# Performance work log

Measured on AMD Instinct MI355X. Metric: run time of the kernel, lower is better.

Reference implementation:

```python
import jax, jax.numpy as jnp
import numpy as np

EPS = 1e-05
H, N, F = 1024, 16, 4096  # hidden_dim, state_dim, ffn_dim


def layernorm(x, g, b):
    mu = jnp.mean(x, axis=-1, keepdims=True)
    var = jnp.mean(jnp.square(x - mu), axis=-1, keepdims=True)
    return (x - mu) * jax.lax.rsqrt(var + EPS) * g + b


def setup_inputs() -> dict:
    key = jax.random.key(0)
    ks = jax.random.split(key, 12)
    B, L = 2, 2048
    s = lambda fan_in: 1.0 / np.sqrt(fan_in)
    inp = {
        "x": jax.random.normal(ks[0], (B, L, H), jnp.float32),
        "ln1_g": jnp.ones((H,), jnp.float32),
        "ln1_b": jnp.zeros((H,), jnp.float32),
        "Wd": jax.random.uniform(ks[1], (H, H), jnp.float32, -s(H), s(H)),
        "bd": jnp.zeros((H,), jnp.float32),
        "Wbc": jax.random.uniform(ks[2], (2 * N, H), jnp.float32, -s(H), s(H)),
        "bbc": jnp.zeros((2 * N,), jnp.float32),
        "A_log": jnp.log(jnp.tile(jnp.arange(1, N + 1, dtype=jnp.float32), (H, 1))),
        "D": jnp.ones((H,), jnp.float32),
        "ln2_g": jnp.ones((H,), jnp.float32),
        "ln2_b": jnp.zeros((H,), jnp.float32),
        "W1": jax.random.uniform(ks[3], (F, H), jnp.float32, -s(H), s(H)),
        "b1": jnp.zeros((F,), jnp.float32),
        "W2": jax.random.uniform(ks[4], (H, F), jnp.float32, -s(F), s(F)),
        "b2": jnp.zeros((H,), jnp.float32),
    }
    return inp


def _selective_ssm(xn, delta, Bm, Cm, A, D):
    # xn: (B,L,H)  delta: (B,L,H)  Bm,Cm: (B,L,N)  A: (H,N)  D: (H,)
    Bsz = xn.shape[0]
    # time-major for scan
    xs = (jnp.moveaxis(delta, 1, 0), jnp.moveaxis(Bm, 1, 0),
          jnp.moveaxis(Cm, 1, 0), jnp.moveaxis(xn, 1, 0))

    def step(h, t):
        d_t, b_t, c_t, x_t = t  # (B,H), (B,N), (B,N), (B,H)
        dA = jnp.exp(d_t[:, :, None] * A)                      # (B,H,N)
        dBx = d_t[:, :, None] * b_t[:, None, :] * x_t[:, :, None]
        h = dA * h + dBx                                       # (B,H,N)
        y = jnp.einsum('bhn,bn->bh', h, c_t)                   # (B,H)
        return h, y

    h0 = jnp.zeros((Bsz, H, N), xn.dtype)
    _, ys = jax.lax.scan(step, h0, xs)
    y = jnp.moveaxis(ys, 0, 1)  # (B,L,H)
    return y + D * xn


def reference(x, ln1_g, ln1_b, Wd, bd, Wbc, bbc, A_log, D,
              ln2_g, ln2_b, W1, b1, W2, b2):
    # --- SSMLayer: pre-norm selective SSM + residual ---
    xn = layernorm(x, ln1_g, ln1_b)
    delta = jax.nn.softplus(xn @ Wd.T + bd)      # (B,L,H)
    bc = xn @ Wbc.T + bbc                        # (B,L,2N)
    Bm, Cm = bc[..., :N], bc[..., N:]
    A = -jnp.exp(A_log)                          # (H,N), negative real
    ssm_out = x + _selective_ssm(xn, delta, Bm, Cm, A, D)
    # --- MambaBlock: norm -> FFN -> residual with ssm_out ---
    normed = layernorm(ssm_out, ln2_g, ln2_b)
    hff = jax.nn.gelu(normed @ W1.T + b1, approximate=False)
    ffn_out = hff @ W2.T + b2
    return ffn_out + ssm_out
```

## Files before the change

### kernel.cpp

```cpp
#include <hip/hip_runtime.h>
#include <cstdint>
#include <cstddef>

typedef unsigned short USHORT;
typedef __bf16 bf16x8 __attribute__((ext_vector_type(8)));
typedef float f32x4 __attribute__((ext_vector_type(4)));

__device__ __forceinline__ float b2f(USHORT u) {
    union { unsigned int i; float f; } v; v.i = ((unsigned int)u) << 16; return v.f;
}
__device__ __forceinline__ USHORT f2bf(float f) {
    union { float f; unsigned int i; } v; v.f = f;
    unsigned int u = v.i;
    unsigned int r = (u + 0x7FFFu + ((u >> 16) & 1u)) >> 16;
    return (USHORT)r;
}
__device__ __forceinline__ float fexp2(float x) { return __builtin_amdgcn_exp2f(x); }

__device__ __forceinline__ void gload_lds16(const void* g, void* l) {
    __builtin_amdgcn_global_load_lds(
        (const __attribute__((address_space(1))) void*)(uintptr_t)g,
        (__attribute__((address_space(3))) void*)(uint32_t)(uintptr_t)l,
        16, 0, 0);
}

__global__ __launch_bounds__(256)
void f2b_kernel(const float* __restrict__ src, USHORT* __restrict__ dst, int n)
{
    int i = (blockIdx.x * 256 + threadIdx.x) * 4;
    if (i < n) {
        float4 v = *(const float4*)(src + i);
        ushort4 o;
        o.x = f2bf(v.x); o.y = f2bf(v.y); o.z = f2bf(v.z); o.w = f2bf(v.w);
        *(ushort4*)(dst + i) = o;
    }
}

__global__ __launch_bounds__(256)
void ln_kernel(const float* __restrict__ inp, const float* __restrict__ g,
               const float* __restrict__ bsh, USHORT* __restrict__ out)
{
    const int tid = threadIdx.x;
    const size_t row = blockIdx.x;
    float4 t = ((const float4*)inp)[row * 256 + tid];
    float v[4] = { t.x, t.y, t.z, t.w };
    float s = v[0] + v[1] + v[2] + v[3];
    float sq = v[0]*v[0] + v[1]*v[1] + v[2]*v[2] + v[3]*v[3];
    #pragma unroll
    for (int off = 32; off; off >>= 1) { s += __shfl_down(s, off); sq += __shfl_down(sq, off); }
    __shared__ float red[8];
    const int wv = tid >> 6;
    if ((tid & 63) == 0) { red[wv] = s; red[wv + 4] = sq; }
    __syncthreads();
    const float S  = red[0] + red[1] + red[2] + red[3];
    const float SQ = red[4] + red[5] + red[6] + red[7];
    const float mu = S * (1.0f / 1024.0f);
    const float var = SQ * (1.0f / 1024.0f) - mu * mu;
    const float rs = rsqrtf(var + 1e-5f);
    float4 gv = ((const float4*)g)[tid];
    float4 bv = ((const float4*)bsh)[tid];
    ushort4 o;
    o.x = f2bf((v[0] - mu) * rs * gv.x + bv.x);
    o.y = f2bf((v[1] - mu) * rs * gv.y + bv.y);
    o.z = f2bf((v[2] - mu) * rs * gv.z + bv.z);
    o.w = f2bf((v[3] - mu) * rs * gv.w + bv.w);
    ((ushort4*)out)[row * 256 + tid] = o;
}

template<int EPI>
__global__ __launch_bounds__(256)
void gemm_bt(const USHORT* __restrict__ A, const USHORT* __restrict__ B,
             const float* __restrict__ bias, void* __restrict__ outp,
             void* __restrict__ outp2, int M, int N, int K, int lda, int ldb)
{
    __shared__ __align__(16) unsigned char smem[32768];
    USHORT* As = (USHORT*)smem;
    USHORT* Bs = (USHORT*)(smem + 8192);
    const int tid = threadIdx.x;
    const int lane = tid & 63;
    const int w = tid >> 6;
    const int wr = w >> 1, wc = w & 1;

    const int nx = gridDim.x, ny = gridDim.y;
    const int pid = blockIdx.y * nx + blockIdx.x;
    const int npg = 8 * nx;
    const int gid = pid / npg;
    const int first = gid * 8;
    const int rem = ny - first;
    const int gsz = (rem < 8) ? rem : 8;
    const int py = first + (pid % npg) % gsz;
    const int px = (pid % npg) / gsz;
    const int tm = py * 128;
    const int tn = px * 128;

    USHORT* po = nullptr;
    if constexpr (EPI == 3) {
        const int z = blockIdx.z;
        A += (size_t)z * K;
        B += (size_t)z * K;
        po = ((z < 2) ? (USHORT*)outp : (USHORT*)outp2) + (size_t)(z & 1) * M * N;
    }

    f32x4 acc[4][4];
    #pragma unroll
    for (int i = 0; i < 4; i++)
        #pragma unroll
        for (int j = 0; j < 4; j++) acc[i][j] = (f32x4){0.f, 0.f, 0.f, 0.f};

    const int srow = tid >> 2;
    const int scol = (tid & 3) * 8;
    const USHORT* gA0 = A + (size_t)(tm + srow) * lda + scol;
    const USHORT* gA1 = A + (size_t)(tm + 64 + srow) * lda + scol;
    const USHORT* gB0 = B + (size_t)(tn + srow) * ldb + scol;
    const USHORT* gB1 = B + (size_t)(tn + 64 + srow) * ldb + scol;
    USHORT* lA0 = As + w * 512;
    USHORT* lA1 = As + 2048 + w * 512;
    USHORT* lB0 = Bs + w * 512;
    USHORT* lB1 = Bs + 2048 + w * 512;

    const int fr = lane & 15;
    const int fko = (lane >> 4) * 8;
    const int quad = lane >> 4;

    for (int k0 = 0; k0 < K; k0 += 64) {
        gload_lds16(gA0 + k0, lA0);
        gload_lds16(gA1 + k0, lA1);
        gload_lds16(gB0 + k0, lB0);
        gload_lds16(gB1 + k0, lB1);
        gload_lds16(gA0 + k0 + 32, lA0 + 8192);
        gload_lds16(gA1 + k0 + 32, lA1 + 8192);
        gload_lds16(gB0 + k0 + 32, lB0 + 8192);
        gload_lds16(gB1 + k0 + 32, lB1 + 8192);
        __syncthreads();
        #pragma unroll
        for (int h = 0; h < 2; h++) {
            const USHORT* Ah = As + h * 8192;
            const USHORT* Bh = Bs + h * 8192;
            bf16x8 af[4], bfr[4];
            #pragma unroll
            for (int i = 0; i < 4; i++) {
                af[i]  = *(const bf16x8*)(Ah + (wr * 64 + i * 16 + fr) * 32 + fko);
                bfr[i] = *(const bf16x8*)(Bh + (wc * 64 + i * 16 + fr) * 32 + fko);
            }
            #pragma unroll
            for (int i = 0; i < 4; i++)
                #pragma unroll
                for (int j = 0; j < 4; j++)
                    acc[i][j] = __builtin_amdgcn_mfma_f32_16x16x32_bf16(af[i], bfr[j], acc[i][j], 0, 0, 0);
        }
        __syncthreads();
    }

    float* eW = (float*)(smem + (size_t)w * 4352);
    const int rr = lane >> 5;
    const int cc = lane & 31;
    const int gcolb = tn + wc * 64;
    float2 bvv;
    if constexpr (EPI == 3) { bvv.x = 0.f; bvv.y = 0.f; }
    else bvv = *(const float2*)&bias[gcolb + cc * 2];

    #pragma unroll
    for (int i = 0; i < 4; i++) {
        #pragma unroll
        for (int j = 0; j < 4; j++)
            #pragma unroll
            for (int r = 0; r < 4; r++)
                eW[(quad * 4 + r) * 68 + j * 16 + fr] = acc[i][j][r];
        __syncthreads();
        const int grow0 = tm + wr * 64 + i * 16;
        #pragma unroll
        for (int rp = 0; rp < 8; rp++) {
            const int row = rp * 2 + rr;
            const float2 v = *(const float2*)&eW[row * 68 + cc * 2];
            const size_t gidx = (size_t)(grow0 + row) * N + gcolb + cc * 2;
            if constexpr (EPI == 1) {
                const float z0 = v.x + bvv.x, z1 = v.y + bvv.y;
                const float u0 = z0 * (0.7978845608f + 0.035677408f * z0 * z0);
                const float u1 = z1 * (0.7978845608f + 0.035677408f * z1 * z1);
                const float s0 = __builtin_amdgcn_rcpf(1.f + fexp2(2.885390082f * u0));
                const float s1 = __builtin_amdgcn_rcpf(1.f + fexp2(2.885390082f * u1));
                const float g0 = z0 * (1.f - s0), g1 = z1 * (1.f - s1);
                const uint32_t pk = (uint32_t)f2bf(g0) | ((uint32_t)f2bf(g1) << 16);
                *(uint32_t*)((USHORT*)outp + gidx) = pk;
            } else {
                const uint32_t pk = (uint32_t)f2bf(v.x) | ((uint32_t)f2bf(v.y) << 16);
                *(uint32_t*)(po + gidx) = pk;
            }
        }
        __syncthreads();
    }
}

__global__ __launch_bounds__(256)
void delta_reduce(const USHORT* __restrict__ p, const float* __restrict__ bias,
                  float* __restrict__ out)
{
    const size_t PS = (size_t)4096 * 1024;
    const size_t i = ((size_t)blockIdx.x * 256 + threadIdx.x) * 4;
    ushort4 a = *(const ushort4*)(p + i);
    ushort4 b = *(const ushort4*)(p + PS + i);
    float4 bv = *(const float4*)(bias + (i & 1023));
    float z[4] = { b2f(a.x) + b2f(b.x) + bv.x, b2f(a.y) + b2f(b.y) + bv.y,
                   b2f(a.z) + b2f(b.z) + bv.z, b2f(a.w) + b2f(b.w) + bv.w };
    float4 o;
    o.x = (z[0] > 20.f) ? z[0] : 0.69314718f * __log2f(1.f + fexp2(z[0] * 1.44269504f));
    o.y = (z[1] > 20.f) ? z[1] : 0.69314718f * __log2f(1.f + fexp2(z[1] * 1.44269504f));
    o.z = (z[2] > 20.f) ? z[2] : 0.69314718f * __log2f(1.f + fexp2(z[2] * 1.44269504f));
    o.w = (z[3] > 20.f) ? z[3] : 0.69314718f * __log2f(1.f + fexp2(z[3] * 1.44269504f));
    *(float4*)(out + i) = o;
}

__global__ __launch_bounds__(256)
void ffn2_reduce(const USHORT* __restrict__ p01, const USHORT* __restrict__ p23,
                 const float* __restrict__ bias, const float* __restrict__ extra,
                 float* __restrict__ out)
{
    const size_t PS = (size_t)4096 * 1024;
    const size_t i = ((size_t)blockIdx.x * 256 + threadIdx.x) * 4;
    ushort4 a = *(const ushort4*)(p01 + i);
    ushort4 b = *(const ushort4*)(p01 + PS + i);
    ushort4 c = *(const ushort4*)(p23 + i);
    ushort4 d = *(const ushort4*)(p23 + PS + i);
    float4 bv = *(const float4*)(bias + (i & 1023));
    float4 ev = *(const float4*)(extra + i);
    float4 o;
    o.x = b2f(a.x) + b2f(b.x) + b2f(c.x) + b2f(d.x) + bv.x + ev.x;
    o.y = b2f(a.y) + b2f(b.y) + b2f(c.y) + b2f(d.y) + bv.y + ev.y;
    o.z = b2f(a.z) + b2f(b.z) + b2f(c.z) + b2f(d.z) + bv.z + ev.z;
    o.w = b2f(a.w) + b2f(b.w) + b2f(c.w) + b2f(d.w) + bv.w + ev.w;
    *(float4*)(out + i) = o;
}

__global__ __launch_bounds__(256)
void bc_mfma(const USHORT* __restrict__ xn, const USHORT* __restrict__ WbcB,
             const float* __restrict__ bbc, float* __restrict__ bc)
{
    __shared__ __align__(16) USHORT As[64 * 32];
    __shared__ __align__(16) USHORT Bs[32 * 32];
    const int tid = threadIdx.x;
    const int lane = tid & 63;
    const int w = tid >> 6;
    const int tok0 = blockIdx.x * 64;

    const int srow = tid >> 2;
    const int scol = (tid & 3) * 8;
    const USHORT* gA = xn + (size_t)(tok0 + srow) * 1024 + scol;
    const USHORT* gB = WbcB + (size_t)srow * 1024 + scol;
    USHORT* lA = As + w * 512;
    USHORT* lB = Bs + w * 512;

    const int fr = lane & 15;
    const int fko = (lane >> 4) * 8;
    const int quad = lane >> 4;

    f32x4 acc[2];
    acc[0] = (f32x4){0.f, 0.f, 0.f, 0.f};
    acc[1] = (f32x4){0.f, 0.f, 0.f, 0.f};

    for (int k0 = 0; k0 < 1024; k0 += 32) {
        gload_lds16(gA + k0, lA);
        if (w < 2) gload_lds16(gB + k0, lB);
        __syncthreads();
        bf16x8 af = *(const bf16x8*)(As + (w * 16 + fr) * 32 + fko);
        bf16x8 b0 = *(const bf16x8*)(Bs + (fr) * 32 + fko);
        bf16x8 b1 = *(const bf16x8*)(Bs + (16 + fr) * 32 + fko);
        acc[0] = __builtin_amdgcn_mfma_f32_16x16x32_bf16(af, b0, acc[0], 0, 0, 0);
        acc[1] = __builtin_amdgcn_mfma_f32_16x16x32_bf16(af, b1, acc[1], 0, 0, 0);
        __syncthreads();
    }

    #pragma unroll
    for (int j = 0; j < 2; j++) {
        const int col = j * 16 + fr;
        const float bv = bbc[col];
        #pragma unroll
        for (int r = 0; r < 4; r++) {
            const int row = tok0 + w * 16 + quad * 4 + r;
            bc[(size_t)row * 32 + col] = acc[j][r] + bv;
        }
    }
}

#define SCAN_P 64
#define SCAN_T 32

__global__ __launch_bounds__(256)
void scan_pass1(const USHORT* __restrict__ xn, const float* __restrict__ delta,
                const float* __restrict__ bc, const float* __restrict__ Alog,
                float* __restrict__ sEnd, float* __restrict__ Ptot)
{
    const int tid = threadIdx.x;
    const int h = blockIdx.x * 256 + tid;
    const int b = blockIdx.y;
    const int p = blockIdx.z;
    const size_t tok0 = (size_t)b * 2048 + p * SCAN_T;

    __shared__ __align__(16) float sBC[SCAN_T][32];
    {
        int t = tid >> 3, q = (tid & 7) * 4;
        *(float4*)&sBC[t][q] = *(const float4*)(bc + (tok0 + t) * 32 + q);
    }

    float en[16], s[16], P[16];
    #pragma unroll
    for (int k = 0; k < 4; k++) {
        float4 a = *(const float4*)(Alog + h * 16 + k * 4);
        en[k*4+0] = -__expf(a.x) * 1.44269504f;
        en[k*4+1] = -__expf(a.y) * 1.44269504f;
        en[k*4+2] = -__expf(a.z) * 1.44269504f;
        en[k*4+3] = -__expf(a.w) * 1.44269504f;
    }
    #pragma unroll
    for (int n = 0; n < 16; n++) { s[n] = 0.f; P[n] = 1.f; }
    __syncthreads();

    const float* dp = delta + tok0 * 1024 + h;
    const USHORT* xp = xn + tok0 * 1024 + h;
    float d_c = dp[0];
    USHORT x_c = xp[0];
    for (int t = 0; t < SCAN_T; ++t) {
        const int tn = (t < SCAN_T - 1) ? t + 1 : t;
        float d_n = dp[(size_t)tn * 1024];
        USHORT x_n = xp[(size_t)tn * 1024];
        const float dx = d_c * b2f(x_c);
        #pragma unroll
        for (int k = 0; k < 4; k++) {
            float4 Bv = *(const float4*)&sBC[t][k*4];
            float bb[4] = { Bv.x, Bv.y, Bv.z, Bv.w };
            #pragma unroll
            for (int j = 0; j < 4; j++) {
                const int n = k*4 + j;
                const float dA = fexp2(d_c * en[n]);
                s[n] = fmaf(dA, s[n], dx * bb[j]);
                P[n] *= dA;
            }
        }
        d_c = d_n; x_c = x_n;
    }

    const size_t off = (size_t)p * 32768 + ((size_t)b * 1024 + h) * 16;
    #pragma unroll
    for (int k = 0; k < 4; k++) {
        *(float4*)(sEnd + off + k*4) = (float4){ s[k*4], s[k*4+1], s[k*4+2], s[k*4+3] };
        *(float4*)(Ptot + off + k*4) = (float4){ P[k*4], P[k*4+1], P[k*4+2], P[k*4+3] };
    }
}

__global__ __launch_bounds__(256)
void scan_mid(const float* __restrict__ sEnd, const float* __restrict__ Ptot,
              float* __restrict__ sIn)
{
    const int L = blockIdx.x * 256 + threadIdx.x;
    float s = 0.f;
    #pragma unroll 8
    for (int p = 0; p < SCAN_P; ++p) {
        const size_t off = (size_t)p * 32768 + L;
        sIn[off] = s;
        s = fmaf(Ptot[off], s, sEnd[off]);
    }
}

__global__ __launch_bounds__(256)
void scan_pass2(const float* __restrict__ x, const USHORT* __restrict__ xn,
                const float* __restrict__ delta, const float* __restrict__ bc,
                const float* __restrict__ Alog, const float* __restrict__ Dp,
                const float* __restrict__ sIn, float* __restrict__ ssm)
{
    const int tid = threadIdx.x;
    const int h = blockIdx.x * 256 + tid;
    const int b = blockIdx.y;
    const int p = blockIdx.z;
    const size_t tok0 = (size_t)b * 2048 + p * SCAN_T;

    __shared__ __align__(16) float sBC[SCAN_T][32];
    {
        int t = tid >> 3, q = (tid & 7) * 4;
        *(float4*)&sBC[t][q] = *(const float4*)(bc + (tok0 + t) * 32 + q);
    }

    float en[16], s[16];
    #pragma unroll
    for (int k = 0; k < 4; k++) {
        float4 a = *(const float4*)(Alog + h * 16 + k * 4);
        en[k*4+0] = -__expf(a.x) * 1.44269504f;
        en[k*4+1] = -__expf(a.y) * 1.44269504f;
        en[k*4+2] = -__expf(a.z) * 1.44269504f;
        en[k*4+3] = -__expf(a.w) * 1.44269504f;
    }
    const size_t off = (size_t)p * 32768 + ((size_t)b * 1024 + h) * 16;
    #pragma unroll
    for (int k = 0; k < 4; k++) {
        float4 v = *(const float4*)(sIn + off + k*4);
        s[k*4] = v.x; s[k*4+1] = v.y; s[k*4+2] = v.z; s[k*4+3] = v.w;
    }
    const float Dv = Dp[h];
    __syncthreads();

    const float* dp = delta + tok0 * 1024 + h;
    const USHORT* xp = xn + tok0 * 1024 + h;
    const float* xrp = x + tok0 * 1024 + h;
    float* op = ssm + tok0 * 1024 + h;

    float d_c = dp[0];
    USHORT x_c = xp[0];
    float xr_c = xrp[0];
    for (int t = 0; t < SCAN_T; ++t) {
        const int tn = (t < SCAN_T - 1) ? t + 1 : t;
        float d_n = dp[(size_t)tn * 1024];
        USHORT x_n = xp[(size_t)tn * 1024];
        float xr_n = xrp[(size_t)tn * 1024];
        const float xv = b2f(x_c);
        const float dx = d_c * xv;
        float y = 0.f;
        #pragma unroll
        for (int k = 0; k < 4; k++) {
            float4 Bv = *(const float4*)&sBC[t][k*4];
            float4 Cv = *(const float4*)&sBC[t][16 + k*4];
            float bb[4] = { Bv.x, Bv.y, Bv.z, Bv.w };
            float cc[4] = { Cv.x, Cv.y, Cv.z, Cv.w };
            #pragma unroll
            for (int j = 0; j < 4; j++) {
                const int n = k*4 + j;
                const float dA = fexp2(d_c * en[n]);
                s[n] = fmaf(dA, s[n], dx * bb[j]);
                y = fmaf(cc[j], s[n], y);
            }
        }
        op[(size_t)t * 1024] = xr_c + y + Dv * xv;
        d_c = d_n; x_c = x_n; xr_c = xr_n;
    }
}

extern "C" void kernel_launch(void* const* d_in, const int* in_sizes, int n_in,
                              void* d_out, int out_size, void* d_ws, size_t ws_size,
                              hipStream_t stream)
{
    const float* x    = (const float*)d_in[0];
    const float* ln1g = (const float*)d_in[1];
    const float* ln1b = (const float*)d_in[2];
    const float* Wd   = (const float*)d_in[3];
    const float* bd   = (const float*)d_in[4];
    const float* Wbc  = (const float*)d_in[5];
    const float* bbc  = (const float*)d_in[6];
    const float* Alog = (const float*)d_in[7];
    const float* Dp   = (const float*)d_in[8];
    const float* ln2g = (const float*)d_in[9];
    const float* ln2b = (const float*)d_in[10];
    const float* W1   = (const float*)d_in[11];
    const float* b1   = (const float*)d_in[12];
    const float* W2   = (const float*)d_in[13];
    const float* b2   = (const float*)d_in[14];
    float* out = (float*)d_out;

    char* ws = (char*)d_ws;
    const size_t MB = 1024 * 1024;
    float*  deltaW = (float*)(ws + 0);
    float*  ssmW   = (float*)(ws + 16 * MB);
    USHORT* xnW    = (USHORT*)(ws + 32 * MB);
    USHORT* nrmW   = (USHORT*)(ws + 40 * MB);
    USHORT* hffW   = (USHORT*)(ws + 48 * MB);
    float*  bcW    = (float*)(ws + 80 * MB);
    USHORT* WdB    = (USHORT*)(ws + 81 * MB);
    USHORT* W1B    = (USHORT*)(ws + 83 * MB);
    USHORT* W2B    = (USHORT*)(ws + 91 * MB);
    USHORT* WbcB   = (USHORT*)(ws + 99 * MB);
    USHORT* dpart  = (USHORT*)(ws + 48 * MB);
    float*  sEndW  = (float*)(ws + 48 * MB);
    float*  PtotW  = (float*)(ws + 56 * MB);
    float*  sInW   = (float*)(ws + 64 * MB);
    USHORT* ffn2p01 = (USHORT*)(ws + 0);
    USHORT* ffn2p23 = (USHORT*)(ws + 32 * MB);

    f2b_kernel<<<1024, 256, 0, stream>>>(Wd, WdB, 1024 * 1024);
    f2b_kernel<<<4096, 256, 0, stream>>>(W1, W1B, 4096 * 1024);
    f2b_kernel<<<4096, 256, 0, stream>>>(W2, W2B, 1024 * 4096);
    f2b_kernel<<<32, 256, 0, stream>>>(Wbc, WbcB, 32 * 1024);
    ln_kernel<<<4096, 256, 0, stream>>>(x, ln1g, ln1b, xnW);
    gemm_bt<3><<<dim3(8, 32, 2), 256, 0, stream>>>(xnW, WdB, nullptr, dpart, nullptr, 4096, 1024, 512, 1024, 1024);
    delta_reduce<<<4096, 256, 0, stream>>>(dpart, bd, deltaW);
    bc_mfma<<<64, 256, 0, stream>>>(xnW, WbcB, bbc, bcW);
    scan_pass1<<<dim3(4, 2, SCAN_P), 256, 0, stream>>>(xnW, deltaW, bcW, Alog, sEndW, PtotW);
    scan_mid<<<128, 256, 0, stream>>>(sEndW, PtotW, sInW);
    scan_pass2<<<dim3(4, 2, SCAN_P), 256, 0, stream>>>(x, xnW, deltaW, bcW, Alog, Dp, sInW, ssmW);
    ln_kernel<<<4096, 256, 0, stream>>>(ssmW, ln2g, ln2b, nrmW);
    gemm_bt<1><<<dim3(32, 32), 256, 0, stream>>>(nrmW, W1B, b1, hffW, nullptr, 4096, 4096, 1024, 1024, 1024);
    gemm_bt<3><<<dim3(8, 32, 4), 256, 0, stream>>>(hffW, W2B, nullptr, ffn2p01, ffn2p23, 4096, 1024, 1024, 4096, 4096);
    ffn2_reduce<<<4096, 256, 0, stream>>>(ffn2p01, ffn2p23, b2, ssmW, out);

    (void)in_sizes; (void)n_in; (void)out_size; (void)ws_size;
}
```

Before: 333.3 us.

## Store split-K partials in MFMA fragment layout and merge weight conversion launches

The split-K GEMM epilogue no longer stages accumulators through LDS with block barriers. Each lane writes its accumulators as packed bf16 pairs straight into a tiled, fragment-ordered buffer. The delta and FFN2 reduce kernels are rewritten to decode that tiled layout, and the four weight-conversion launches become one kernel. The GELU epilogue also drops its per-block barriers, since each wave only touches its own LDS region. In return, the reduce kernels read 32-bit words of which they use only one 16-bit half, relying on cache reuse between neighbouring rows.

```diff
diff --git a/kernel.cpp b/kernel.cpp
--- a/kernel.cpp
+++ b/kernel.cpp
@@ -25,15 +25,22 @@
 }
 
 __global__ __launch_bounds__(256)
-void f2b_kernel(const float* __restrict__ src, USHORT* __restrict__ dst, int n)
-{
-    int i = (blockIdx.x * 256 + threadIdx.x) * 4;
-    if (i < n) {
-        float4 v = *(const float4*)(src + i);
-        ushort4 o;
-        o.x = f2bf(v.x); o.y = f2bf(v.y); o.z = f2bf(v.z); o.w = f2bf(v.w);
-        *(ushort4*)(dst + i) = o;
-    }
+void f2b_all(const float* __restrict__ Wd, const float* __restrict__ W1,
+             const float* __restrict__ W2, const float* __restrict__ Wbc,
+             USHORT* __restrict__ WdB, USHORT* __restrict__ W1B,
+             USHORT* __restrict__ W2B, USHORT* __restrict__ WbcB)
+{
+    const int bid = blockIdx.x;
+    const float* src; USHORT* dst; int off;
+    if (bid < 1024)      { src = Wd;  dst = WdB;  off = bid; }
+    else if (bid < 5120) { src = W1;  dst = W1B;  off = bid - 1024; }
+    else if (bid < 9216) { src = W2;  dst = W2B;  off = bid - 5120; }
+    else                 { src = Wbc; dst = WbcB; off = bid - 9216; }
+    const int i = (off * 256 + threadIdx.x) * 4;
+    float4 v = *(const float4*)(src + i);
+    ushort4 o;
+    o.x = f2bf(v.x); o.y = f2bf(v.y); o.z = f2bf(v.z); o.w = f2bf(v.w);
+    *(ushort4*)(dst + i) = o;
 }
 
 __global__ __launch_bounds__(256)
@@ -93,12 +100,13 @@
     const int tm = py * 128;
     const int tn = px * 128;
 
-    USHORT* po = nullptr;
+    uint32_t* po = nullptr;
     if constexpr (EPI == 3) {
         const int z = blockIdx.z;
         A += (size_t)z * K;
         B += (size_t)z * K;
-        po = ((z < 2) ? (USHORT*)outp : (USHORT*)outp2) + (size_t)(z & 1) * M * N;
+        USHORT* p16 = ((z < 2) ? (USHORT*)outp : (USHORT*)outp2) + (size_t)(z & 1) * M * N;
+        po = (uint32_t*)p16;
     }
 
     f32x4 acc[4][4];
@@ -151,29 +159,40 @@
         __syncthreads();
     }
 
-    float* eW = (float*)(smem + (size_t)w * 4352);
-    const int rr = lane >> 5;
-    const int cc = lane & 31;
-    const int gcolb = tn + wc * 64;
-    float2 bvv;
-    if constexpr (EPI == 3) { bvv.x = 0.f; bvv.y = 0.f; }
-    else bvv = *(const float2*)&bias[gcolb + cc * 2];
-
-    #pragma unroll
-    for (int i = 0; i < 4; i++) {
-        #pragma unroll
-        for (int j = 0; j < 4; j++)
-            #pragma unroll
-            for (int r = 0; r < 4; r++)
-                eW[(quad * 4 + r) * 68 + j * 16 + fr] = acc[i][j][r];
-        __syncthreads();
-        const int grow0 = tm + wr * 64 + i * 16;
-        #pragma unroll
-        for (int rp = 0; rp < 8; rp++) {
-            const int row = rp * 2 + rr;
-            const float2 v = *(const float2*)&eW[row * 68 + cc * 2];
-            const size_t gidx = (size_t)(grow0 + row) * N + gcolb + cc * 2;
-            if constexpr (EPI == 1) {
+    if constexpr (EPI == 3) {
+        const int Nt = N >> 4;
+        #pragma unroll
+        for (int i = 0; i < 4; i++) {
+            const int i16 = (tm >> 4) + wr * 4 + i;
+            #pragma unroll
+            for (int j = 0; j < 4; j++) {
+                const int j16 = (tn >> 4) + wc * 4 + j;
+                uint32_t* base = po + ((size_t)(i16 * Nt + j16) * 2) * 64 + lane;
+                base[0]  = (uint32_t)f2bf(acc[i][j][0]) | ((uint32_t)f2bf(acc[i][j][1]) << 16);
+                base[64] = (uint32_t)f2bf(acc[i][j][2]) | ((uint32_t)f2bf(acc[i][j][3]) << 16);
+            }
+        }
+        return;
+    } else {
+        float* eW = (float*)(smem + (size_t)w * 4352);
+        const int rr = lane >> 5;
+        const int cc = lane & 31;
+        const int gcolb = tn + wc * 64;
+        float2 bvv = *(const float2*)&bias[gcolb + cc * 2];
+
+        #pragma unroll
+        for (int i = 0; i < 4; i++) {
+            #pragma unroll
+            for (int j = 0; j < 4; j++)
+                #pragma unroll
+                for (int r = 0; r < 4; r++)
+                    eW[(quad * 4 + r) * 68 + j * 16 + fr] = acc[i][j][r];
+            const int grow0 = tm + wr * 64 + i * 16;
+            #pragma unroll
+            for (int rp = 0; rp < 8; rp++) {
+                const int row = rp * 2 + rr;
+                const float2 v = *(const float2*)&eW[row * 68 + cc * 2];
+                const size_t gidx = (size_t)(grow0 + row) * N + gcolb + cc * 2;
                 const float z0 = v.x + bvv.x, z1 = v.y + bvv.y;
                 const float u0 = z0 * (0.7978845608f + 0.035677408f * z0 * z0);
                 const float u1 = z1 * (0.7978845608f + 0.035677408f * z1 * z1);
@@ -182,53 +201,67 @@
                 const float g0 = z0 * (1.f - s0), g1 = z1 * (1.f - s1);
                 const uint32_t pk = (uint32_t)f2bf(g0) | ((uint32_t)f2bf(g1) << 16);
                 *(uint32_t*)((USHORT*)outp + gidx) = pk;
-            } else {
-                const uint32_t pk = (uint32_t)f2bf(v.x) | ((uint32_t)f2bf(v.y) << 16);
-                *(uint32_t*)(po + gidx) = pk;
             }
         }
-        __syncthreads();
-    }
-}
-
-__global__ __launch_bounds__(256)
-void delta_reduce(const USHORT* __restrict__ p, const float* __restrict__ bias,
+    }
+}
+
+__device__ __forceinline__ float exhalf(uint32_t v, int hf) {
+    union { unsigned int i; float f; } u;
+    u.i = hf ? (v & 0xFFFF0000u) : (v << 16);
+    return u.f;
+}
+
+__global__ __launch_bounds__(256)
+void delta_reduce(const uint32_t* __restrict__ p, const float* __restrict__ bias,
                   float* __restrict__ out)
 {
-    const size_t PS = (size_t)4096 * 1024;
-    const size_t i = ((size_t)blockIdx.x * 256 + threadIdx.x) * 4;
-    ushort4 a = *(const ushort4*)(p + i);
-    ushort4 b = *(const ushort4*)(p + PS + i);
-    float4 bv = *(const float4*)(bias + (i & 1023));
-    float z[4] = { b2f(a.x) + b2f(b.x) + bv.x, b2f(a.y) + b2f(b.y) + bv.y,
-                   b2f(a.z) + b2f(b.z) + bv.z, b2f(a.w) + b2f(b.w) + bv.w };
+    const size_t PS = (size_t)4096 * 1024 / 2;
+    const size_t e0 = ((size_t)blockIdx.x * 256 + threadIdx.x) * 4;
+    const int row = (int)(e0 >> 10);
+    const int col = (int)(e0 & 1023);
+    const int i16 = row >> 4, j16 = col >> 4;
+    const int quad = (row >> 2) & 3, rp = (row >> 1) & 1, hf = row & 1;
+    const size_t base = (((size_t)(i16 * 64 + j16) * 2 + rp) << 6) + (quad * 16 + (col & 15));
+    uint4 a = *(const uint4*)(p + base);
+    uint4 b = *(const uint4*)(p + PS + base);
+    float4 bv = *(const float4*)(bias + col);
+    float z[4] = { exhalf(a.x, hf) + exhalf(b.x, hf) + bv.x,
+                   exhalf(a.y, hf) + exhalf(b.y, hf) + bv.y,
+                   exhalf(a.z, hf) + exhalf(b.z, hf) + bv.z,
+                   exhalf(a.w, hf) + exhalf(b.w, hf) + bv.w };
     float4 o;
     o.x = (z[0] > 20.f) ? z[0] : 0.69314718f * __log2f(1.f + fexp2(z[0] * 1.44269504f));
     o.y = (z[1] > 20.f) ? z[1] : 0.69314718f * __log2f(1.f + fexp2(z[1] * 1.44269504f));
     o.z = (z[2] > 20.f) ? z[2] : 0.69314718f * __log2f(1.f + fexp2(z[2] * 1.44269504f));
     o.w = (z[3] > 20.f) ? z[3] : 0.69314718f * __log2f(1.f + fexp2(z[3] * 1.44269504f));
-    *(float4*)(out + i) = o;
-}
-
-__global__ __launch_bounds__(256)
-void ffn2_reduce(const USHORT* __restrict__ p01, const USHORT* __restrict__ p23,
+    *(float4*)(out + e0) = o;
+}
+
+__global__ __launch_bounds__(256)
+void ffn2_reduce(const uint32_t* __restrict__ p01, const uint32_t* __restrict__ p23,
                  const float* __restrict__ bias, const float* __restrict__ extra,
                  float* __restrict__ out)
 {
-    const size_t PS = (size_t)4096 * 1024;
-    const size_t i = ((size_t)blockIdx.x * 256 + threadIdx.x) * 4;
-    ushort4 a = *(const ushort4*)(p01 + i);
-    ushort4 b = *(const ushort4*)(p01 + PS + i);
-    ushort4 c = *(const ushort4*)(p23 + i);
-    ushort4 d = *(const ushort4*)(p23 + PS + i);
-    float4 bv = *(const float4*)(bias + (i & 1023));
-    float4 ev = *(const float4*)(extra + i);
+    const size_t PS = (size_t)4096 * 1024 / 2;
+    const size_t e0 = ((size_t)blockIdx.x * 256 + threadIdx.x) * 4;
+    const int row = (int)(e0 >> 10);
+    const int col = (int)(e0 & 1023);
+    const int i16 = row >> 4, j16 = col >> 4;
+    const int quad = (row >> 2) & 3, rp = (row >> 1) & 1, hf = row & 1;
+    const size_t base = (((size_t)(i16 * 64 + j16) * 2 + rp) << 6) + (quad * 16 + (col & 15));
+    uint4 a = *(const uint4*)(p01 + base);
+    uint4 b = *(const uint4*)(p01 + PS + base);
+    uint4 c = *(const uint4*)(p23 + base);
+    uint4 d = *(const uint4*)(p23 + PS + base);
+    float4 bv = *(const float4*)(bias + col);
+    float4 ev = *(const float4*)(extra + e0);
     float4 o;
-    o.x = b2f(a.x) + b2f(b.x) + b2f(c.x) + b2f(d.x) + bv.x + ev.x;
-    o.y = b2f(a.y) + b2f(b.y) + b2f(c.y) + b2f(d.y) + bv.y + ev.y;
-    o.z = b2f(a.z) + b2f(b.z) + b2f(c.z) + b2f(d.z) + bv.z + ev.z;
-    o.w = b2f(a.w) + b2f(b.w) + b2f(c.w) + b2f(d.w) + bv.w + ev.w;
-    *(float4*)(out + i) = o;
+    o.x = exhalf(a.x,hf)+exhalf(b.x,hf)+exhalf(c.x,hf)+exhalf(d.x,hf) + bv.x + ev.x;
+    o.y = exhalf(a.y,hf)+exhalf(b.y,hf)+exhalf(c.y,hf)+exhalf(d.y,hf) + bv.y + ev.y;
+    o.z = exhalf(a.z,hf)+exhalf(b.z,hf)+exhalf(c.z,hf)+exhalf(d.z,hf) + bv.z + ev.z;
+    o.w = exhalf(a.w,hf)+exhalf(b.w,hf)+exhalf(c.w,hf)+exhalf(d.w,hf) + bv.w + ev.w;
+    *(float4*)(out + e0) = o;
 }
 
 __global__ __launch_bounds__(256)
@@ -471,13 +504,10 @@
     USHORT* ffn2p01 = (USHORT*)(ws + 0);
     USHORT* ffn2p23 = (USHORT*)(ws + 32 * MB);
 
-    f2b_kernel<<<1024, 256, 0, stream>>>(Wd, WdB, 1024 * 1024);
-    f2b_kernel<<<4096, 256, 0, stream>>>(W1, W1B, 4096 * 1024);
-    f2b_kernel<<<4096, 256, 0, stream>>>(W2, W2B, 1024 * 4096);
-    f2b_kernel<<<32, 256, 0, stream>>>(Wbc, WbcB, 32 * 1024);
+    f2b_all<<<9248, 256, 0, stream>>>(Wd, W1, W2, Wbc, WdB, W1B, W2B, WbcB);
     ln_kernel<<<4096, 256, 0, stream>>>(x, ln1g, ln1b, xnW);
     gemm_bt<3><<<dim3(8, 32, 2), 256, 0, stream>>>(xnW, WdB, nullptr, dpart, nullptr, 4096, 1024, 512, 1024, 1024);
-    delta_reduce<<<4096, 256, 0, stream>>>(dpart, bd, deltaW);
+    delta_reduce<<<4096, 256, 0, stream>>>((const uint32_t*)dpart, bd, deltaW);
     bc_mfma<<<64, 256, 0, stream>>>(xnW, WbcB, bbc, bcW);
     scan_pass1<<<dim3(4, 2, SCAN_P), 256, 0, stream>>>(xnW, deltaW, bcW, Alog, sEndW, PtotW);
     scan_mid<<<128, 256, 0, stream>>>(sEndW, PtotW, sInW);
@@ -485,7 +515,7 @@
     ln_kernel<<<4096, 256, 0, stream>>>(ssmW, ln2g, ln2b, nrmW);
     gemm_bt<1><<<dim3(32, 32), 256, 0, stream>>>(nrmW, W1B, b1, hffW, nullptr, 4096, 4096, 1024, 1024, 1024);
     gemm_bt<3><<<dim3(8, 32, 4), 256, 0, stream>>>(hffW, W2B, nullptr, ffn2p01, ffn2p23, 4096, 1024, 1024, 4096, 4096);
-    ffn2_reduce<<<4096, 256, 0, stream>>>(ffn2p01, ffn2p23, b2, ssmW, out);
+    ffn2_reduce<<<4096, 256, 0, stream>>>((const uint32_t*)ffn2p01, (const uint32_t*)ffn2p23, b2, ssmW, out);
 
     (void)in_sizes; (void)n_in; (void)out_size; (void)ws_size;
 }
```

Measured after the change: 337.8 us. About the same (+1.4%).

## Switch GEMM to 32x32x16 MFMA tiles and merge weight conversion launches

Applied to the files above, without the earlier changes.

The GEMM inner loop now uses 32x32x16 bf16 MFMA with 2x2 accumulator tiles per wave instead of 4x4 tiles of 16x16x32. This cuts LDS fragment reads per MFMA and the instruction count. The epilogue is rewritten for the new accumulator layout with a padded per-wave staging buffer, and the block-wide barriers are removed. The four fp32-to-bf16 weight conversion launches are fused into one kernel to save launch overhead.

```diff
diff --git a/kernel.cpp b/kernel.cpp
--- a/kernel.cpp
+++ b/kernel.cpp
@@ -5,6 +5,7 @@
 typedef unsigned short USHORT;
 typedef __bf16 bf16x8 __attribute__((ext_vector_type(8)));
 typedef float f32x4 __attribute__((ext_vector_type(4)));
+typedef float f32x16 __attribute__((ext_vector_type(16)));
 
 __device__ __forceinline__ float b2f(USHORT u) {
     union { unsigned int i; float f; } v; v.i = ((unsigned int)u) << 16; return v.f;
@@ -25,15 +26,22 @@
 }
 
 __global__ __launch_bounds__(256)
-void f2b_kernel(const float* __restrict__ src, USHORT* __restrict__ dst, int n)
-{
-    int i = (blockIdx.x * 256 + threadIdx.x) * 4;
-    if (i < n) {
-        float4 v = *(const float4*)(src + i);
-        ushort4 o;
-        o.x = f2bf(v.x); o.y = f2bf(v.y); o.z = f2bf(v.z); o.w = f2bf(v.w);
-        *(ushort4*)(dst + i) = o;
-    }
+void f2b_all(const float* __restrict__ Wd, const float* __restrict__ W1,
+             const float* __restrict__ W2, const float* __restrict__ Wbc,
+             USHORT* __restrict__ WdB, USHORT* __restrict__ W1B,
+             USHORT* __restrict__ W2B, USHORT* __restrict__ WbcB)
+{
+    const int bid = blockIdx.x;
+    const float* src; USHORT* dst; int off;
+    if (bid < 1024)      { src = Wd;  dst = WdB;  off = bid; }
+    else if (bid < 5120) { src = W1;  dst = W1B;  off = bid - 1024; }
+    else if (bid < 9216) { src = W2;  dst = W2B;  off = bid - 5120; }
+    else                 { src = Wbc; dst = WbcB; off = bid - 9216; }
+    const int i = (off * 256 + threadIdx.x) * 4;
+    float4 v = *(const float4*)(src + i);
+    ushort4 o;
+    o.x = f2bf(v.x); o.y = f2bf(v.y); o.z = f2bf(v.z); o.w = f2bf(v.w);
+    *(ushort4*)(dst + i) = o;
 }
 
 __global__ __launch_bounds__(256)
@@ -80,6 +88,8 @@
     const int lane = tid & 63;
     const int w = tid >> 6;
     const int wr = w >> 1, wc = w & 1;
+    const int l31 = lane & 31;
+    const int lh  = lane >> 5;
 
     const int nx = gridDim.x, ny = gridDim.y;
     const int pid = blockIdx.y * nx + blockIdx.x;
@@ -101,11 +111,13 @@
         po = ((z < 2) ? (USHORT*)outp : (USHORT*)outp2) + (size_t)(z & 1) * M * N;
     }
 
-    f32x4 acc[4][4];
-    #pragma unroll
-    for (int i = 0; i < 4; i++)
-        #pragma unroll
-        for (int j = 0; j < 4; j++) acc[i][j] = (f32x4){0.f, 0.f, 0.f, 0.f};
+    f32x16 acc[2][2];
+    #pragma unroll
+    for (int i = 0; i < 2; i++)
+        #pragma unroll
+        for (int j = 0; j < 2; j++)
+            #pragma unroll
+            for (int r = 0; r < 16; r++) acc[i][j][r] = 0.f;
 
     const int srow = tid >> 2;
     const int scol = (tid & 3) * 8;
@@ -118,10 +130,6 @@
     USHORT* lB0 = Bs + w * 512;
     USHORT* lB1 = Bs + 2048 + w * 512;
 
-    const int fr = lane & 15;
-    const int fko = (lane >> 4) * 8;
-    const int quad = lane >> 4;
-
     for (int k0 = 0; k0 < K; k0 += 64) {
         gload_lds16(gA0 + k0, lA0);
         gload_lds16(gA1 + k0, lA1);
@@ -133,61 +141,64 @@
         gload_lds16(gB1 + k0 + 32, lB1 + 8192);
         __syncthreads();
         #pragma unroll
-        for (int h = 0; h < 2; h++) {
-            const USHORT* Ah = As + h * 8192;
-            const USHORT* Bh = Bs + h * 8192;
-            bf16x8 af[4], bfr[4];
-            #pragma unroll
-            for (int i = 0; i < 4; i++) {
-                af[i]  = *(const bf16x8*)(Ah + (wr * 64 + i * 16 + fr) * 32 + fko);
-                bfr[i] = *(const bf16x8*)(Bh + (wc * 64 + i * 16 + fr) * 32 + fko);
-            }
-            #pragma unroll
-            for (int i = 0; i < 4; i++)
+        for (int h2 = 0; h2 < 2; h2++) {
+            const USHORT* Ah = As + h2 * 8192;
+            const USHORT* Bh = Bs + h2 * 8192;
+            bf16x8 af[2][2], bfr[2][2];
+            #pragma unroll
+            for (int i = 0; i < 2; i++)
                 #pragma unroll
-                for (int j = 0; j < 4; j++)
-                    acc[i][j] = __builtin_amdgcn_mfma_f32_16x16x32_bf16(af[i], bfr[j], acc[i][j], 0, 0, 0);
+                for (int c = 0; c < 2; c++) {
+                    af[i][c]  = *(const bf16x8*)(Ah + (wr * 64 + i * 32 + l31) * 32 + c * 16 + lh * 8);
+                    bfr[i][c] = *(const bf16x8*)(Bh + (wc * 64 + i * 32 + l31) * 32 + c * 16 + lh * 8);
+                }
+            #pragma unroll
+            for (int c = 0; c < 2; c++)
+                #pragma unroll
+                for (int i = 0; i < 2; i++)
+                    #pragma unroll
+                    for (int j = 0; j < 2; j++)
+                        acc[i][j] = __builtin_amdgcn_mfma_f32_32x32x16_bf16(af[i][c], bfr[j][c], acc[i][j], 0, 0, 0);
         }
         __syncthreads();
     }
 
     float* eW = (float*)(smem + (size_t)w * 4352);
-    const int rr = lane >> 5;
-    const int cc = lane & 31;
-    const int gcolb = tn + wc * 64;
-    float2 bvv;
-    if constexpr (EPI == 3) { bvv.x = 0.f; bvv.y = 0.f; }
-    else bvv = *(const float2*)&bias[gcolb + cc * 2];
-
-    #pragma unroll
-    for (int i = 0; i < 4; i++) {
-        #pragma unroll
-        for (int j = 0; j < 4; j++)
-            #pragma unroll
-            for (int r = 0; r < 4; r++)
-                eW[(quad * 4 + r) * 68 + j * 16 + fr] = acc[i][j][r];
-        __syncthreads();
-        const int grow0 = tm + wr * 64 + i * 16;
-        #pragma unroll
-        for (int rp = 0; rp < 8; rp++) {
-            const int row = rp * 2 + rr;
-            const float2 v = *(const float2*)&eW[row * 68 + cc * 2];
-            const size_t gidx = (size_t)(grow0 + row) * N + gcolb + cc * 2;
-            if constexpr (EPI == 1) {
-                const float z0 = v.x + bvv.x, z1 = v.y + bvv.y;
-                const float u0 = z0 * (0.7978845608f + 0.035677408f * z0 * z0);
-                const float u1 = z1 * (0.7978845608f + 0.035677408f * z1 * z1);
-                const float s0 = __builtin_amdgcn_rcpf(1.f + fexp2(2.885390082f * u0));
-                const float s1 = __builtin_amdgcn_rcpf(1.f + fexp2(2.885390082f * u1));
-                const float g0 = z0 * (1.f - s0), g1 = z1 * (1.f - s1);
-                const uint32_t pk = (uint32_t)f2bf(g0) | ((uint32_t)f2bf(g1) << 16);
-                *(uint32_t*)((USHORT*)outp + gidx) = pk;
-            } else {
-                const uint32_t pk = (uint32_t)f2bf(v.x) | ((uint32_t)f2bf(v.y) << 16);
-                *(uint32_t*)(po + gidx) = pk;
+    const int cc = lane & 15;
+    const int rr = lane >> 4;
+
+    #pragma unroll
+    for (int i = 0; i < 2; i++) {
+        #pragma unroll
+        for (int j = 0; j < 2; j++) {
+            #pragma unroll
+            for (int r = 0; r < 16; r++)
+                eW[((r & 3) + 8 * (r >> 2) + 4 * lh) * 33 + l31] = acc[i][j][r];
+            const int grow0 = tm + wr * 64 + i * 32;
+            const int gcol0 = tn + wc * 64 + j * 32;
+            float2 bvv;
+            if constexpr (EPI == 3) { bvv.x = 0.f; bvv.y = 0.f; }
+            else bvv = *(const float2*)&bias[gcol0 + cc * 2];
+            #pragma unroll
+            for (int p = 0; p < 8; p++) {
+                const int row = p * 4 + rr;
+                const float2 v = *(const float2*)&eW[row * 33 + cc * 2];
+                const size_t gidx = (size_t)(grow0 + row) * N + gcol0 + cc * 2;
+                if constexpr (EPI == 1) {
+                    const float z0 = v.x + bvv.x, z1 = v.y + bvv.y;
+                    const float u0 = z0 * (0.7978845608f + 0.035677408f * z0 * z0);
+                    const float u1 = z1 * (0.7978845608f + 0.035677408f * z1 * z1);
+                    const float s0 = __builtin_amdgcn_rcpf(1.f + fexp2(2.885390082f * u0));
+                    const float s1 = __builtin_amdgcn_rcpf(1.f + fexp2(2.885390082f * u1));
+                    const float g0 = z0 * (1.f - s0), g1 = z1 * (1.f - s1);
+                    const uint32_t pk = (uint32_t)f2bf(g0) | ((uint32_t)f2bf(g1) << 16);
+                    *(uint32_t*)((USHORT*)outp + gidx) = pk;
+                } else {
+                    const uint32_t pk = (uint32_t)f2bf(v.x) | ((uint32_t)f2bf(v.y) << 16);
+                    *(uint32_t*)(po + gidx) = pk;
+                }
             }
         }
-        __syncthreads();
     }
 }
 
@@ -471,10 +482,7 @@
     USHORT* ffn2p01 = (USHORT*)(ws + 0);
     USHORT* ffn2p23 = (USHORT*)(ws + 32 * MB);
 
-    f2b_kernel<<<1024, 256, 0, stream>>>(Wd, WdB, 1024 * 1024);
-    f2b_kernel<<<4096, 256, 0, stream>>>(W1, W1B, 4096 * 1024);
-    f2b_kernel<<<4096, 256, 0, stream>>>(W2, W2B, 1024 * 4096);
-    f2b_kernel<<<32, 256, 0, stream>>>(Wbc, WbcB, 32 * 1024);
+    f2b_all<<<9248, 256, 0, stream>>>(Wd, W1, W2, Wbc, WdB, W1B, W2B, WbcB);
     ln_kernel<<<4096, 256, 0, stream>>>(x, ln1g, ln1b, xnW);
     gemm_bt<3><<<dim3(8, 32, 2), 256, 0, stream>>>(xnW, WdB, nullptr, dpart, nullptr, 4096, 1024, 512, 1024, 1024);
     delta_reduce<<<4096, 256, 0, stream>>>(dpart, bd, deltaW);
```

After: 344.6 us. 3.4% more time.
